# Performance work log

Hardware: AMD Instinct MI355X
Metric: run time of the kernel (lower is better)

Reference implementation:

```python
import jax, jax.numpy as jnp
import numpy as np
from jax import lax

STRIDES = (8, 16, 32)
FEAT_SIZES = ((80, 80), (40, 40), (20, 20))  # 640x640 input
NUM_CLASSES = 80
NMS_THR = 0.65
SCORE_THR = 0.01
NMS_PRE = 1000
MAX_PER_IMG = 100


def make_points():
    # MlvlPointGenerator.grid_priors with offset=0, with_stride=True.
    pts = []
    for (h, w), s in zip(FEAT_SIZES, STRIDES):
        y, x = jnp.meshgrid(jnp.arange(h, dtype=jnp.float32),
                            jnp.arange(w, dtype=jnp.float32), indexing='ij')
        pts.append(jnp.stack([x.ravel() * s, y.ravel() * s,
                              jnp.full(h * w, float(s)),
                              jnp.full(h * w, float(s))], axis=-1))
    return jnp.concatenate(pts, axis=0)  # [P, 4] = (px, py, sx, sy)


def decode_boxes(points, reg):
    # YOLOXBBoxDecoder: xy = reg[:2]*stride + point; wh = exp(reg[2:])*stride
    xys = reg[..., :2] * points[..., 2:] + points[..., :2]
    whs = jnp.exp(reg[..., 2:]) * points[..., 2:]
    half = whs * 0.5
    return jnp.concatenate([xys - half, xys + half], axis=-1)  # [..., 4] xyxy


def pairwise_iou(b):
    # b: [N, 4] xyxy
    area = (b[:, 2] - b[:, 0]) * (b[:, 3] - b[:, 1])
    lt = jnp.maximum(b[:, None, :2], b[None, :, :2])
    rb = jnp.minimum(b[:, None, 2:], b[None, :, 2:])
    wh = jnp.clip(rb - lt, 0.0)
    inter = wh[..., 0] * wh[..., 1]
    return inter / (area[:, None] + area[None, :] - inter + 1e-9)


def nms_image(cls_s, boxes, obj):
    # cls_s: [P, C] sigmoid scores, boxes: [P, 4], obj: [P] sigmoid objectness
    max_scores = jnp.max(cls_s, axis=-1)
    labels = jnp.argmax(cls_s, axis=-1)
    scores = max_scores * obj
    masked = jnp.where(scores >= SCORE_THR, scores, -1.0)
    top_scores, top_idx = lax.top_k(masked, NMS_PRE)  # sorted descending
    valid = top_scores >= SCORE_THR
    b = boxes[top_idx]            # [K, 4]
    lab = labels[top_idx]         # [K]
    # batched_nms: offset boxes per class so cross-class boxes never overlap
    off = lab.astype(b.dtype)[:, None] * (jnp.max(jnp.abs(b)) + 1.0)
    iou = pairwise_iou(b + off)   # [K, K]
    idx = jnp.arange(NMS_PRE)

    def body(i, keep):
        sup = (iou[i] > NMS_THR) & keep[i] & (idx > i)
        return keep & ~sup

    keep = lax.fori_loop(0, NMS_PRE, body, valid)
    # compact kept detections (score-sorted order preserved), pad to MAX_PER_IMG
    order = jnp.argsort(~keep, stable=True)[:MAX_PER_IMG]
    k = keep[order]
    out_b = jnp.where(k[:, None], b[order], 0.0)
    out_s = jnp.where(k, top_scores[order], 0.0)
    out_l = jnp.where(k, lab[order], -1)
    return out_b, out_s, out_l


def setup_inputs() -> dict:
    key = jax.random.key(0)
    ks = jax.random.split(key, 9)
    shapes = {
        'cls0': (32, NUM_CLASSES, 80, 80), 'cls1': (32, NUM_CLASSES, 40, 40),
        'cls2': (32, NUM_CLASSES, 20, 20),
        'reg0': (32, 4, 80, 80), 'reg1': (32, 4, 40, 40), 'reg2': (32, 4, 20, 20),
        'obj0': (32, 1, 80, 80), 'obj1': (32, 1, 40, 40), 'obj2': (32, 1, 20, 20),
    }
    return {n: jax.random.normal(k, s, dtype=jnp.float32)
            for (n, s), k in zip(shapes.items(), ks)}


def reference(cls0, cls1, cls2, reg0, reg1, reg2, obj0, obj1, obj2):
    def flat(xs, c):
        return jnp.concatenate(
            [jnp.transpose(x, (0, 2, 3, 1)).reshape(x.shape[0], -1, c) for x in xs],
            axis=1)
    cls = flat([cls0, cls1, cls2], NUM_CLASSES)   # [N, P, C]
    reg = flat([reg0, reg1, reg2], 4)             # [N, P, 4]
    obj = flat([obj0, obj1, obj2], 1)[..., 0]     # [N, P]
    points = make_points()                        # [P, 4]
    boxes = decode_boxes(points[None], reg)       # [N, P, 4]
    cls = jax.nn.sigmoid(cls)
    obj = jax.nn.sigmoid(obj)
    return jax.vmap(nms_image)(cls, boxes, obj)   # ([N,M,4],[N,M],[N,M] labels)
```

## Files before the change

kernel.cpp:

```cpp
#include <hip/hip_runtime.h>
#include <stdint.h>

#define N_IMG 32
#define P_TOT 8400
#define NCLS 80
#define NMS_PRE 1000
#define MAXOUT 100
#define SCORE_THRF 0.01f
#define NMS_THRF 0.65f
#define CAND_N 2048
#define NB 512
#define BINBASE 8192


__device__ __forceinline__ float sigmoidf_(float x) { return 1.0f / (1.0f + expf(-x)); }

__global__ __launch_bounds__(256) void k_score(
    const float* __restrict__ cls0, const float* __restrict__ cls1, const float* __restrict__ cls2,
    const float* __restrict__ obj0, const float* __restrict__ obj1, const float* __restrict__ obj2,
    uint64_t* __restrict__ keys)
{
    __shared__ uint64_t part[4][64];
    int lane = threadIdx.x & 63, wid = threadIdx.x >> 6;
    int a = blockIdx.x * 64 + lane;
    int n = a / P_TOT;
    int p = a - n * P_TOT;

    const float* cl; const float* ob; int HW, q;
    if (p < 6400)      { cl = cls0; ob = obj0; HW = 6400; q = p; }
    else if (p < 8000) { cl = cls1; ob = obj1; HW = 1600; q = p - 6400; }
    else               { cl = cls2; ob = obj2; HW = 400;  q = p - 8000; }

    const float* cbase = cl + (size_t)n * NCLS * HW + q;
    uint64_t m = 0;
    int c0 = wid * 20;
    #pragma unroll
    for (int i = 0; i < 20; ++i) {
        int c = c0 + i;
        float s = sigmoidf_(cbase[(size_t)c * HW]);
        uint64_t pk = ((uint64_t)__float_as_uint(s) << 8) | (uint32_t)(79 - c);
        m = m > pk ? m : pk;
    }
    part[wid][lane] = m;
    __syncthreads();

    if (wid == 0) {
        uint64_t m0 = part[0][lane], m1 = part[1][lane];
        uint64_t m2 = part[2][lane], m3 = part[3][lane];
        uint64_t ma = m0 > m1 ? m0 : m1, mb = m2 > m3 ? m2 : m3;
        uint64_t mm = ma > mb ? ma : mb;
        float best = __uint_as_float((uint32_t)(mm >> 8));
        int bc = 79 - (int)(mm & 0xFFu);

        float so = sigmoidf_(ob[(size_t)n * HW + q]);
        float sc = __fmul_rn(best, so);
        float masked = (sc >= SCORE_THRF) ? sc : -1.0f;
        uint32_t u = __float_as_uint(masked);
        uint32_t ord = (u & 0x80000000u) ? ~u : (u | 0x80000000u);
        uint32_t dk = ~ord;
        keys[a] = ((uint64_t)dk << 32) | (uint32_t)((p << 8) | bc);
    }
}

__global__ __launch_bounds__(1024) void k_select(
    const uint64_t* __restrict__ keys,
    const float* __restrict__ reg0, const float* __restrict__ reg1, const float* __restrict__ reg2,
    float* __restrict__ out)
{
    __shared__ __align__(16) char big[44032];
    __shared__ uint64_t cand[CAND_N];
    __shared__ float    fsh[17];
    __shared__ int      s_misc[2];
    __shared__ int      kidx[MAXOUT];

    uint32_t* hist    = (uint32_t*)big;
    uint32_t* base    = (uint32_t*)(big + 2048);
    uint32_t* fill    = (uint32_t*)(big + 4096);
    uint64_t* grouped = (uint64_t*)(big + 8192);
    float4* s_obx = (float4*)big;
    float4* s_raw = (float4*)(big + 16000);
    float2* s_sl  = (float2*)(big + 32000);
    float*  s_oar = (float*)(big + 40000);

    int n = blockIdx.x, tid = threadIdx.x;

    if (tid < NB) { hist[tid] = 0; fill[tid] = 0; }
    for (int t = tid; t < CAND_N; t += 1024) cand[t] = ~0ull;
    __syncthreads();

    uint64_t rk[9];
    #pragma unroll
    for (int it = 0; it < 9; ++it) {
        int t = tid + it * 1024;
        uint64_t k = ~0ull;
        if (t < P_TOT) {
            k = keys[(size_t)n * P_TOT + t];
            uint32_t dk = (uint32_t)(k >> 32);
            if (!(dk & 0x80000000u)) atomicAdd(&hist[(dk >> 17) - BINBASE], 1u);
        }
        rk[it] = k;
    }
    __syncthreads();

    if (tid < 64) {
        uint32_t c[8]; uint32_t s = 0;
        #pragma unroll
        for (int i = 0; i < 8; ++i) { c[i] = hist[tid * 8 + i]; s += c[i]; }
        uint32_t inc = s;
        #pragma unroll
        for (int o = 1; o < 64; o <<= 1) {
            uint32_t v = __shfl_up(inc, o);
            if (tid >= o) inc += v;
        }
        uint32_t excl = inc - s;
        uint32_t b = excl;
        #pragma unroll
        for (int i = 0; i < 8; ++i) { base[tid * 8 + i] = b; b += c[i]; }
        uint32_t total = __shfl(inc, 63);
        uint32_t target = total < (uint32_t)NMS_PRE ? total : (uint32_t)NMS_PRE;
        uint32_t cum = excl; int found = 0x7fffffff;
        #pragma unroll
        for (int i = 0; i < 8; ++i) {
            cum += c[i];
            if (found == 0x7fffffff && cum >= target && target > 0) found = tid * 8 + i;
        }
        #pragma unroll
        for (int o = 32; o > 0; o >>= 1) { int f = __shfl_xor(found, o); found = f < found ? f : found; }
        if (tid == 0) { s_misc[0] = (total > 0) ? found : -1; s_misc[1] = (int)target; }
    }
    __syncthreads();
    int Bcut = s_misc[0];
    int V    = s_misc[1];

    #pragma unroll
    for (int it = 0; it < 9; ++it) {
        uint64_t k = rk[it];
        uint32_t dk = (uint32_t)(k >> 32);
        if (!(dk & 0x80000000u)) {
            int bin = (int)((dk >> 17) - BINBASE);
            if (bin <= Bcut) {
                uint32_t pos = base[bin] + atomicAdd(&fill[bin], 1u);
                if (pos < CAND_N) grouped[pos] = k;
            }
        }
    }
    __syncthreads();

    int ccnt = 0;
    if (Bcut >= 0) {
        uint32_t cc = base[Bcut] + hist[Bcut];
        ccnt = cc < (uint32_t)CAND_N ? (int)cc : CAND_N;
    }
    for (int s = tid; s < ccnt; s += 1024) {
        uint64_t k = grouped[s];
        uint32_t dk = (uint32_t)(k >> 32);
        int bin = (int)((dk >> 17) - BINBASE);
        uint32_t b0 = base[bin];
        uint32_t e0 = b0 + hist[bin]; if (e0 > (uint32_t)CAND_N) e0 = CAND_N;
        uint32_t r = b0;
        for (uint32_t t = b0; t < e0; ++t) r += (grouped[t] < k) ? 1u : 0u;
        if (r < (uint32_t)CAND_N) cand[r] = k;
    }
    __syncthreads();

    float4 bx = make_float4(0.f, 0.f, 0.f, 0.f);
    float scm = -1.0f, labf = 0.f, m = 0.f;
    if (tid < NMS_PRE) {
        uint64_t key = cand[tid];
        uint32_t dk = (uint32_t)(key >> 32);
        if (!(dk & 0x80000000u)) {
            uint32_t low = (uint32_t)key;
            int lab = (int)(low & 0xFFu);
            int p   = (int)(low >> 8);
            uint32_t ord = ~dk;
            scm = __uint_as_float(ord ^ 0x80000000u);

            const float* rg; int HW, q, W; float s;
            if (p < 6400)      { rg = reg0; HW = 6400; q = p;        W = 80; s = 8.f; }
            else if (p < 8000) { rg = reg1; HW = 1600; q = p - 6400; W = 40; s = 16.f; }
            else               { rg = reg2; HW = 400;  q = p - 8000; W = 20; s = 32.f; }

            float px = (float)(q % W) * s;
            float py = (float)(q / W) * s;
            const float* rb = rg + (size_t)n * 4 * HW + q;
            float dx = rb[0], dy = rb[HW], dw = rb[2 * HW], dh = rb[3 * HW];
            float cx = __fadd_rn(__fmul_rn(dx, s), px);
            float cy = __fadd_rn(__fmul_rn(dy, s), py);
            float hw = __fmul_rn(__fmul_rn(expf(dw), s), 0.5f);
            float hh = __fmul_rn(__fmul_rn(expf(dh), s), 0.5f);
            bx.x = __fsub_rn(cx, hw); bx.y = __fsub_rn(cy, hh);
            bx.z = __fadd_rn(cx, hw); bx.w = __fadd_rn(cy, hh);
            labf = (float)lab;
            m = fmaxf(fmaxf(fabsf(bx.x), fabsf(bx.y)), fmaxf(fabsf(bx.z), fabsf(bx.w)));
        }
    }

    #pragma unroll
    for (int o = 32; o > 0; o >>= 1) m = fmaxf(m, __shfl_xor(m, o));
    if ((tid & 63) == 0) fsh[tid >> 6] = m;
    __syncthreads();
    if (tid == 0) {
        float g = fsh[0];
        #pragma unroll
        for (int w = 1; w < 16; ++w) g = fmaxf(g, fsh[w]);
        fsh[16] = g;
    }
    __syncthreads();
    float gmax = fsh[16];

    if (tid < NMS_PRE) {
        float off = __fmul_rn(labf, __fadd_rn(gmax, 1.0f));
        float x1 = __fadd_rn(bx.x, off), y1 = __fadd_rn(bx.y, off);
        float x2 = __fadd_rn(bx.z, off), y2 = __fadd_rn(bx.w, off);
        s_obx[tid] = make_float4(x1, y1, x2, y2);
        s_oar[tid] = __fmul_rn(__fsub_rn(x2, x1), __fsub_rn(y2, y1));
        s_raw[tid] = bx;
        s_sl[tid]  = make_float2(scm, labf);
    }
    __syncthreads();
    if (tid >= 64) return;

    int lane = tid;
    int count = 0;
    float4 g = make_float4(0.f, 0.f, 0.f, 0.f);
    float  gar = 0.f;
    float k1x1 = 0.f, k1y1 = 0.f, k1x2 = 0.f, k1y2 = 0.f, k1a = 0.f;
    float k2x1 = 0.f, k2y1 = 0.f, k2x2 = 0.f, k2y2 = 0.f, k2a = 0.f;

    for (int i = 0; i < V && count < MAXOUT; ++i) {
        if ((i & 63) == 0) {
            int idx = i + lane; if (idx > V - 1) idx = V - 1;
            g = s_obx[idx]; gar = s_oar[idx];
        }
        int src = i & 63;
        float bx1 = __shfl(g.x, src), by1 = __shfl(g.y, src);
        float bx2 = __shfl(g.z, src), by2 = __shfl(g.w, src);
        float ba  = __shfl(gar,  src);

        bool sup = false;
        int c1 = count < 64 ? count : 64;
        if (lane < c1) {
            float ltx = fmaxf(k1x1, bx1), lty = fmaxf(k1y1, by1);
            float rbx = fminf(k1x2, bx2), rby = fminf(k1y2, by2);
            float w = fmaxf(__fsub_rn(rbx, ltx), 0.f);
            float h = fmaxf(__fsub_rn(rby, lty), 0.f);
            float inter = __fmul_rn(w, h);
            float denom = __fadd_rn(__fsub_rn(__fadd_rn(k1a, ba), inter), 1e-9f);
            sup = (inter / denom > NMS_THRF);
        }
        if (count > 64 && lane < count - 64) {
            float ltx = fmaxf(k2x1, bx1), lty = fmaxf(k2y1, by1);
            float rbx = fminf(k2x2, bx2), rby = fminf(k2y2, by2);
            float w = fmaxf(__fsub_rn(rbx, ltx), 0.f);
            float h = fmaxf(__fsub_rn(rby, lty), 0.f);
            float inter = __fmul_rn(w, h);
            float denom = __fadd_rn(__fsub_rn(__fadd_rn(k2a, ba), inter), 1e-9f);
            sup = sup || (inter / denom > NMS_THRF);
        }
        if (__ballot(sup) == 0ull) {
            if (lane == count)      { k1x1 = bx1; k1y1 = by1; k1x2 = bx2; k1y2 = by2; k1a = ba; }
            if (lane + 64 == count) { k2x1 = bx1; k2y1 = by1; k2x2 = bx2; k2y2 = by2; k2a = ba; }
            if (lane == 0) kidx[count] = i;
            ++count;
        }
    }

    float* ob = out;
    float* os = out + N_IMG * MAXOUT * 4;
    float* ol = os + N_IMG * MAXOUT;
    for (int mi = lane; mi < MAXOUT; mi += 64) {
        int o4 = (n * MAXOUT + mi) * 4;
        if (mi < count) {
            int i = kidx[mi];
            float4 b  = s_raw[i];
            float2 sl = s_sl[i];
            ob[o4 + 0] = b.x; ob[o4 + 1] = b.y; ob[o4 + 2] = b.z; ob[o4 + 3] = b.w;
            os[n * MAXOUT + mi] = sl.x;
            ol[n * MAXOUT + mi] = sl.y;
        } else {
            ob[o4 + 0] = 0.f; ob[o4 + 1] = 0.f; ob[o4 + 2] = 0.f; ob[o4 + 3] = 0.f;
            os[n * MAXOUT + mi] = 0.f;
            ol[n * MAXOUT + mi] = -1.f;
        }
    }
}

extern "C" void kernel_launch(void* const* d_in, const int* in_sizes, int n_in,
                              void* d_out, int out_size, void* d_ws, size_t ws_size,
                              hipStream_t stream)
{
    const float* cls0 = (const float*)d_in[0];
    const float* cls1 = (const float*)d_in[1];
    const float* cls2 = (const float*)d_in[2];
    const float* reg0 = (const float*)d_in[3];
    const float* reg1 = (const float*)d_in[4];
    const float* reg2 = (const float*)d_in[5];
    const float* obj0 = (const float*)d_in[6];
    const float* obj1 = (const float*)d_in[7];
    const float* obj2 = (const float*)d_in[8];

    uint64_t* keys = (uint64_t*)d_ws;
    float* out = (float*)d_out;

    k_score<<<(N_IMG * P_TOT) / 64, 256, 0, stream>>>(
        cls0, cls1, cls2, obj0, obj1, obj2, keys);
    k_select<<<N_IMG, 1024, 0, stream>>>(keys, reg0, reg1, reg2, out);
}
```

Measured before the change: 76.22 us.

## Split top-k selection and NMS into separate kernels with prefetched box loads

Splits k_select so it only writes sorted candidate keys and the valid count to workspace, and moves box decoding and greedy NMS into a new 256-thread kernel. The select kernel now rereads keys from global memory instead of holding 9 uint64 values per thread in registers, which is meant to lower register pressure for the 1024-thread block. The NMS loop now reads the next box from LDS one iteration ahead instead of broadcasting by shuffle, shortening the serial loop's dependency chain. The cost is an extra launch plus a global write and read of 1000 keys per image.

```diff
diff --git a/kernel.cpp b/kernel.cpp
--- a/kernel.cpp
+++ b/kernel.cpp
@@ -64,23 +64,14 @@
 
 __global__ __launch_bounds__(1024) void k_select(
     const uint64_t* __restrict__ keys,
-    const float* __restrict__ reg0, const float* __restrict__ reg1, const float* __restrict__ reg2,
-    float* __restrict__ out)
+    uint64_t* __restrict__ skeys, int* __restrict__ nvalid)
 {
-    __shared__ __align__(16) char big[44032];
+    __shared__ uint32_t hist[NB];
+    __shared__ uint32_t base[NB];
+    __shared__ uint32_t fill[NB];
+    __shared__ uint64_t grouped[CAND_N];
     __shared__ uint64_t cand[CAND_N];
-    __shared__ float    fsh[17];
     __shared__ int      s_misc[2];
-    __shared__ int      kidx[MAXOUT];
-
-    uint32_t* hist    = (uint32_t*)big;
-    uint32_t* base    = (uint32_t*)(big + 2048);
-    uint32_t* fill    = (uint32_t*)(big + 4096);
-    uint64_t* grouped = (uint64_t*)(big + 8192);
-    float4* s_obx = (float4*)big;
-    float4* s_raw = (float4*)(big + 16000);
-    float2* s_sl  = (float2*)(big + 32000);
-    float*  s_oar = (float*)(big + 40000);
 
     int n = blockIdx.x, tid = threadIdx.x;
 
@@ -88,17 +79,14 @@
     for (int t = tid; t < CAND_N; t += 1024) cand[t] = ~0ull;
     __syncthreads();
 
-    uint64_t rk[9];
     #pragma unroll
     for (int it = 0; it < 9; ++it) {
         int t = tid + it * 1024;
-        uint64_t k = ~0ull;
         if (t < P_TOT) {
-            k = keys[(size_t)n * P_TOT + t];
+            uint64_t k = keys[(size_t)n * P_TOT + t];
             uint32_t dk = (uint32_t)(k >> 32);
             if (!(dk & 0x80000000u)) atomicAdd(&hist[(dk >> 17) - BINBASE], 1u);
         }
-        rk[it] = k;
     }
     __syncthreads();
 
@@ -130,17 +118,19 @@
     }
     __syncthreads();
     int Bcut = s_misc[0];
-    int V    = s_misc[1];
 
     #pragma unroll
     for (int it = 0; it < 9; ++it) {
-        uint64_t k = rk[it];
-        uint32_t dk = (uint32_t)(k >> 32);
-        if (!(dk & 0x80000000u)) {
-            int bin = (int)((dk >> 17) - BINBASE);
-            if (bin <= Bcut) {
-                uint32_t pos = base[bin] + atomicAdd(&fill[bin], 1u);
-                if (pos < CAND_N) grouped[pos] = k;
+        int t = tid + it * 1024;
+        if (t < P_TOT) {
+            uint64_t k = keys[(size_t)n * P_TOT + t];
+            uint32_t dk = (uint32_t)(k >> 32);
+            if (!(dk & 0x80000000u)) {
+                int bin = (int)((dk >> 17) - BINBASE);
+                if (bin <= Bcut) {
+                    uint32_t pos = base[bin] + atomicAdd(&fill[bin], 1u);
+                    if (pos < CAND_N) grouped[pos] = k;
+                }
             }
         }
     }
@@ -163,103 +153,120 @@
     }
     __syncthreads();
 
-    float4 bx = make_float4(0.f, 0.f, 0.f, 0.f);
-    float scm = -1.0f, labf = 0.f, m = 0.f;
-    if (tid < NMS_PRE) {
-        uint64_t key = cand[tid];
-        uint32_t dk = (uint32_t)(key >> 32);
-        if (!(dk & 0x80000000u)) {
-            uint32_t low = (uint32_t)key;
-            int lab = (int)(low & 0xFFu);
-            int p   = (int)(low >> 8);
-            uint32_t ord = ~dk;
-            scm = __uint_as_float(ord ^ 0x80000000u);
-
-            const float* rg; int HW, q, W; float s;
-            if (p < 6400)      { rg = reg0; HW = 6400; q = p;        W = 80; s = 8.f; }
-            else if (p < 8000) { rg = reg1; HW = 1600; q = p - 6400; W = 40; s = 16.f; }
-            else               { rg = reg2; HW = 400;  q = p - 8000; W = 20; s = 32.f; }
-
-            float px = (float)(q % W) * s;
-            float py = (float)(q / W) * s;
-            const float* rb = rg + (size_t)n * 4 * HW + q;
-            float dx = rb[0], dy = rb[HW], dw = rb[2 * HW], dh = rb[3 * HW];
-            float cx = __fadd_rn(__fmul_rn(dx, s), px);
-            float cy = __fadd_rn(__fmul_rn(dy, s), py);
-            float hw = __fmul_rn(__fmul_rn(expf(dw), s), 0.5f);
-            float hh = __fmul_rn(__fmul_rn(expf(dh), s), 0.5f);
-            bx.x = __fsub_rn(cx, hw); bx.y = __fsub_rn(cy, hh);
-            bx.z = __fadd_rn(cx, hw); bx.w = __fadd_rn(cy, hh);
-            labf = (float)lab;
-            m = fmaxf(fmaxf(fabsf(bx.x), fabsf(bx.y)), fmaxf(fabsf(bx.z), fabsf(bx.w)));
-        }
+    if (tid < NMS_PRE) skeys[n * NMS_PRE + tid] = cand[tid];
+    if (tid == 0) nvalid[n] = s_misc[1];
+}
+
+__global__ __launch_bounds__(256) void k_nms(
+    const uint64_t* __restrict__ skeys, const int* __restrict__ nvalid,
+    const float* __restrict__ reg0, const float* __restrict__ reg1, const float* __restrict__ reg2,
+    float* __restrict__ out)
+{
+    __shared__ float4 s_obx[NMS_PRE];
+    __shared__ float4 s_raw[NMS_PRE];
+    __shared__ float2 s_sl[NMS_PRE];
+    __shared__ float  s_oar[NMS_PRE];
+    __shared__ float  fsh[4];
+    __shared__ int    kidx[MAXOUT];
+
+    int n = blockIdx.x, tid = threadIdx.x;
+    int lane = tid & 63, wv = tid >> 6;
+    int V = nvalid[n];
+
+    float4 bx4[4]; float scm4[4], lab4[4];
+    float m = 0.f;
+    #pragma unroll
+    for (int it = 0; it < 4; ++it) {
+        int t = tid + it * 256;
+        float4 bx = make_float4(0.f, 0.f, 0.f, 0.f);
+        float scm = -1.0f, labf = 0.f;
+        if (t < NMS_PRE) {
+            uint64_t key = skeys[n * NMS_PRE + t];
+            uint32_t dk = (uint32_t)(key >> 32);
+            if (!(dk & 0x80000000u)) {
+                uint32_t low = (uint32_t)key;
+                int lab = (int)(low & 0xFFu);
+                int p   = (int)(low >> 8);
+                uint32_t ord = ~dk;
+                scm = __uint_as_float(ord ^ 0x80000000u);
+
+                const float* rg; int HW, q, W; float s;
+                if (p < 6400)      { rg = reg0; HW = 6400; q = p;        W = 80; s = 8.f; }
+                else if (p < 8000) { rg = reg1; HW = 1600; q = p - 6400; W = 40; s = 16.f; }
+                else               { rg = reg2; HW = 400;  q = p - 8000; W = 20; s = 32.f; }
+
+                float px = (float)(q % W) * s;
+                float py = (float)(q / W) * s;
+                const float* rb = rg + (size_t)n * 4 * HW + q;
+                float dx = rb[0], dy = rb[HW], dw = rb[2 * HW], dh = rb[3 * HW];
+                float cx = __fadd_rn(__fmul_rn(dx, s), px);
+                float cy = __fadd_rn(__fmul_rn(dy, s), py);
+                float hw = __fmul_rn(__fmul_rn(expf(dw), s), 0.5f);
+                float hh = __fmul_rn(__fmul_rn(expf(dh), s), 0.5f);
+                bx.x = __fsub_rn(cx, hw); bx.y = __fsub_rn(cy, hh);
+                bx.z = __fadd_rn(cx, hw); bx.w = __fadd_rn(cy, hh);
+                labf = (float)lab;
+                m = fmaxf(m, fmaxf(fmaxf(fabsf(bx.x), fabsf(bx.y)), fmaxf(fabsf(bx.z), fabsf(bx.w))));
+            }
+            s_raw[t] = bx;
+            s_sl[t]  = make_float2(scm, labf);
+        }
+        bx4[it] = bx; scm4[it] = scm; lab4[it] = labf;
     }
 
     #pragma unroll
     for (int o = 32; o > 0; o >>= 1) m = fmaxf(m, __shfl_xor(m, o));
-    if ((tid & 63) == 0) fsh[tid >> 6] = m;
-    __syncthreads();
-    if (tid == 0) {
-        float g = fsh[0];
-        #pragma unroll
-        for (int w = 1; w < 16; ++w) g = fmaxf(g, fsh[w]);
-        fsh[16] = g;
-    }
-    __syncthreads();
-    float gmax = fsh[16];
-
-    if (tid < NMS_PRE) {
-        float off = __fmul_rn(labf, __fadd_rn(gmax, 1.0f));
-        float x1 = __fadd_rn(bx.x, off), y1 = __fadd_rn(bx.y, off);
-        float x2 = __fadd_rn(bx.z, off), y2 = __fadd_rn(bx.w, off);
-        s_obx[tid] = make_float4(x1, y1, x2, y2);
-        s_oar[tid] = __fmul_rn(__fsub_rn(x2, x1), __fsub_rn(y2, y1));
-        s_raw[tid] = bx;
-        s_sl[tid]  = make_float2(scm, labf);
+    if (lane == 0) fsh[wv] = m;
+    __syncthreads();
+    float gmax = fmaxf(fmaxf(fsh[0], fsh[1]), fmaxf(fsh[2], fsh[3]));
+
+    #pragma unroll
+    for (int it = 0; it < 4; ++it) {
+        int t = tid + it * 256;
+        if (t < NMS_PRE) {
+            float off = __fmul_rn(lab4[it], __fadd_rn(gmax, 1.0f));
+            float x1 = __fadd_rn(bx4[it].x, off), y1 = __fadd_rn(bx4[it].y, off);
+            float x2 = __fadd_rn(bx4[it].z, off), y2 = __fadd_rn(bx4[it].w, off);
+            s_obx[t] = make_float4(x1, y1, x2, y2);
+            s_oar[t] = __fmul_rn(__fsub_rn(x2, x1), __fsub_rn(y2, y1));
+        }
     }
     __syncthreads();
     if (tid >= 64) return;
 
-    int lane = tid;
     int count = 0;
-    float4 g = make_float4(0.f, 0.f, 0.f, 0.f);
-    float  gar = 0.f;
     float k1x1 = 0.f, k1y1 = 0.f, k1x2 = 0.f, k1y2 = 0.f, k1a = 0.f;
     float k2x1 = 0.f, k2y1 = 0.f, k2x2 = 0.f, k2y2 = 0.f, k2a = 0.f;
 
+    float4 nb = s_obx[0]; float na = s_oar[0];
     for (int i = 0; i < V && count < MAXOUT; ++i) {
-        if ((i & 63) == 0) {
-            int idx = i + lane; if (idx > V - 1) idx = V - 1;
-            g = s_obx[idx]; gar = s_oar[idx];
-        }
-        int src = i & 63;
-        float bx1 = __shfl(g.x, src), by1 = __shfl(g.y, src);
-        float bx2 = __shfl(g.z, src), by2 = __shfl(g.w, src);
-        float ba  = __shfl(gar,  src);
+        float4 cb = nb; float ca = na;
+        int ip = (i + 1 < V) ? i + 1 : i;
+        nb = s_obx[ip]; na = s_oar[ip];
 
         bool sup = false;
         int c1 = count < 64 ? count : 64;
         if (lane < c1) {
-            float ltx = fmaxf(k1x1, bx1), lty = fmaxf(k1y1, by1);
-            float rbx = fminf(k1x2, bx2), rby = fminf(k1y2, by2);
+            float ltx = fmaxf(k1x1, cb.x), lty = fmaxf(k1y1, cb.y);
+            float rbx = fminf(k1x2, cb.z), rby = fminf(k1y2, cb.w);
             float w = fmaxf(__fsub_rn(rbx, ltx), 0.f);
             float h = fmaxf(__fsub_rn(rby, lty), 0.f);
             float inter = __fmul_rn(w, h);
-            float denom = __fadd_rn(__fsub_rn(__fadd_rn(k1a, ba), inter), 1e-9f);
+            float denom = __fadd_rn(__fsub_rn(__fadd_rn(k1a, ca), inter), 1e-9f);
             sup = (inter / denom > NMS_THRF);
         }
         if (count > 64 && lane < count - 64) {
-            float ltx = fmaxf(k2x1, bx1), lty = fmaxf(k2y1, by1);
-            float rbx = fminf(k2x2, bx2), rby = fminf(k2y2, by2);
+            float ltx = fmaxf(k2x1, cb.x), lty = fmaxf(k2y1, cb.y);
+            float rbx = fminf(k2x2, cb.z), rby = fminf(k2y2, cb.w);
             float w = fmaxf(__fsub_rn(rbx, ltx), 0.f);
             float h = fmaxf(__fsub_rn(rby, lty), 0.f);
             float inter = __fmul_rn(w, h);
-            float denom = __fadd_rn(__fsub_rn(__fadd_rn(k2a, ba), inter), 1e-9f);
+            float denom = __fadd_rn(__fsub_rn(__fadd_rn(k2a, ca), inter), 1e-9f);
             sup = sup || (inter / denom > NMS_THRF);
         }
         if (__ballot(sup) == 0ull) {
-            if (lane == count)      { k1x1 = bx1; k1y1 = by1; k1x2 = bx2; k1y2 = by2; k1a = ba; }
-            if (lane + 64 == count) { k2x1 = bx1; k2y1 = by1; k2x2 = bx2; k2y2 = by2; k2a = ba; }
+            if (lane == count)      { k1x1 = cb.x; k1y1 = cb.y; k1x2 = cb.z; k1y2 = cb.w; k1a = ca; }
+            if (lane + 64 == count) { k2x1 = cb.x; k2y1 = cb.y; k2x2 = cb.z; k2y2 = cb.w; k2a = ca; }
             if (lane == 0) kidx[count] = i;
             ++count;
         }
@@ -299,10 +306,13 @@
     const float* obj1 = (const float*)d_in[7];
     const float* obj2 = (const float*)d_in[8];
 
-    uint64_t* keys = (uint64_t*)d_ws;
+    uint64_t* keys  = (uint64_t*)d_ws;
+    uint64_t* skeys = (uint64_t*)((char*)d_ws + (4u << 20));
+    int*     nvalid = (int*)((char*)d_ws + (4u << 20) + (512u << 10));
     float* out = (float*)d_out;
 
     k_score<<<(N_IMG * P_TOT) / 64, 256, 0, stream>>>(
         cls0, cls1, cls2, obj0, obj1, obj2, keys);
-    k_select<<<N_IMG, 1024, 0, stream>>>(keys, reg0, reg1, reg2, out);
+    k_select<<<N_IMG, 1024, 0, stream>>>(keys, skeys, nvalid);
+    k_nms<<<N_IMG, 256, 0, stream>>>(skeys, nvalid, reg0, reg1, reg2, out);
 }
```

Result: no change. 76.68 us (+0.6%).
